# Kernel tuning notes

Hardware: AMD Instinct MI355X
Metric: run time of the kernel (lower is better)

## Reference

```python
import jax, jax.numpy as jnp
import numpy as np

B, T, D, H = 64, 256, 512, 512
COMB = D + H + D  # x, h, mask concatenated


def setup_inputs() -> dict:
    key = jax.random.key(0)
    ks = jax.random.split(key, 16)
    s = 1.0 / np.sqrt(COMB)
    sd = 1.0 / np.sqrt(D)
    inp = {
        "x": jax.random.normal(ks[0], (B, 4, T, D), dtype=jnp.float32),
        "X_mean": jax.random.normal(ks[1], (T, D), dtype=jnp.float32),
        # gate linears: stored as [in, out] so we do comb @ W + b
        "Wi": jax.random.uniform(ks[2], (COMB, H), minval=-s, maxval=s),
        "bi": jax.random.uniform(ks[3], (H,), minval=-s, maxval=s),
        "Wf": jax.random.uniform(ks[4], (COMB, H), minval=-s, maxval=s),
        "bf": jax.random.uniform(ks[5], (H,), minval=-s, maxval=s),
        "Wo": jax.random.uniform(ks[6], (COMB, H), minval=-s, maxval=s),
        "bo": jax.random.uniform(ks[7], (H,), minval=-s, maxval=s),
        "Wc": jax.random.uniform(ks[8], (COMB, H), minval=-s, maxval=s),
        "bc": jax.random.uniform(ks[9], (H,), minval=-s, maxval=s),
        # gamma_x_l: FilterLinear with identity filter -> diagonal weight + bias
        "gx_w": jax.random.uniform(ks[10], (D,), minval=-sd, maxval=sd),
        "gx_b": jax.random.uniform(ks[11], (D,), minval=-sd, maxval=sd),
        # gamma_h_l: full linear D -> D, stored [in, out]
        "gh_W": jax.random.uniform(ks[12], (D, D), minval=-sd, maxval=sd),
        "gh_b": jax.random.uniform(ks[13], (D,), minval=-sd, maxval=sd),
    }
    return inp


def _forward(x, X_mean, Wi, bi, Wf, bf, Wo, bo, Wc, bc, gx_w, gx_b, gh_W, gh_b):
    # split the packed input: each [T, B, D] for scan
    X = jnp.transpose(x[:, 0], (1, 0, 2))
    Xl = jnp.transpose(x[:, 1], (1, 0, 2))
    M = jnp.transpose(x[:, 2], (1, 0, 2))
    Dl = jnp.transpose(x[:, 3], (1, 0, 2))

    h0 = jnp.zeros((x.shape[0], H), dtype=x.dtype)
    c0 = jnp.zeros((x.shape[0], H), dtype=x.dtype)

    def step(carry, inp):
        h, c = carry
        xt, xl, m, dl, xm = inp  # xm: [D]
        delta_x = jnp.exp(-jnp.maximum(0.0, dl * gx_w + gx_b))
        delta_h = jnp.exp(-jnp.maximum(0.0, dl @ gh_W + gh_b))
        xt = m * xt + (1.0 - m) * (delta_x * xl + (1.0 - delta_x) * xm)
        h = delta_h * h
        comb = jnp.concatenate([xt, h, m], axis=-1)  # [B, COMB]
        i = jax.nn.sigmoid(comb @ Wi + bi)
        f = jax.nn.sigmoid(comb @ Wf + bf)
        o = jax.nn.sigmoid(comb @ Wo + bo)
        c_tilde = jnp.tanh(comb @ Wc + bc)
        c = f * c + i * c_tilde
        h = o * jnp.tanh(c)
        return (h, c), h

    _, outs = jax.lax.scan(step, (h0, c0), (X, Xl, M, Dl, X_mean))
    return jnp.transpose(outs, (1, 0, 2))  # [B, T, H]


def reference(x, X_mean, Wi, bi, Wf, bf, Wo, bo, Wc, bc, gx_w, gx_b, gh_W, gh_b):
    return _forward(x, X_mean, Wi, bi, Wf, bf, Wo, bo, Wc, bc, gx_w, gx_b, gh_W, gh_b)
```

## Files before the change

kernel.cpp:

```cpp
#include <hip/hip_runtime.h>
#include <hip/hip_fp16.h>
#include <math.h>

#define TT 256
#define BB 64
#define DD 512
#define HH 512
#define NC 2048

#define AH_OFF   0ull
#define DLH_OFF  8388608ull
#define DH_OFF   12582912ull
#define GP_OFF   20971520ull
#define WCT_OFF  37748736ull
#define GHT_OFF  38797312ull
#define WHT_OFF  38928384ull
#define BC_OFF   39452672ull
#define HS_OFF   39454720ull
#define FLG_OFF  39487488ull

typedef _Float16 h8_t __attribute__((ext_vector_type(8)));
typedef _Float16 h4_t __attribute__((ext_vector_type(4)));
typedef float f32x4 __attribute__((ext_vector_type(4)));
typedef unsigned long long ull2_t __attribute__((ext_vector_type(2)));

typedef const __attribute__((address_space(1))) void* gas_p;
typedef __attribute__((address_space(3))) void* las_p;

__device__ __forceinline__ float fast_exp2(float x) {
#if defined(__has_builtin)
#if __has_builtin(__builtin_amdgcn_exp2f)
  return __builtin_amdgcn_exp2f(x);
#else
  return exp2f(x);
#endif
#else
  return exp2f(x);
#endif
}
__device__ __forceinline__ float fast_rcp(float x) {
#if defined(__has_builtin)
#if __has_builtin(__builtin_amdgcn_rcpf)
  return __builtin_amdgcn_rcpf(x);
#else
  return 1.0f / x;
#endif
#else
  return 1.0f / x;
#endif
}
#define LOG2E 1.4426950408889634f
__device__ __forceinline__ float sigmoidf_(float v) {
  return fast_rcp(1.0f + fast_exp2(-LOG2E * v));
}
__device__ __forceinline__ float tanhf_(float v) {
  return 1.0f - 2.0f * fast_rcp(1.0f + fast_exp2(2.0f * LOG2E * v));
}

__global__ __launch_bounds__(256) void repack_kernel(
    const float* __restrict__ Wi, const float* __restrict__ bi,
    const float* __restrict__ Wf, const float* __restrict__ bff,
    const float* __restrict__ Wo, const float* __restrict__ bo,
    const float* __restrict__ Wc, const float* __restrict__ bc,
    const float* __restrict__ ghW,
    __half* __restrict__ WCT, __half* __restrict__ WHT,
    __half* __restrict__ GHT, float* __restrict__ BC) {
  int idx = blockIdx.x * 256 + threadIdx.x;
  int k = idx >> 9, j = idx & 511;
  const float* Ws[4] = {Wi, Wf, Wo, Wc};
  const float* bs[4] = {bi, bff, bo, bc};
#pragma unroll
  for (int g = 0; g < 4; ++g) {
    const float* W = Ws[g];
    int col = j * 4 + g;
    WCT[(size_t)col * 1024 + k] = __float2half(W[(size_t)k * 512 + j]);
    WCT[(size_t)col * 1024 + 512 + k] = __float2half(W[(size_t)(1024 + k) * 512 + j]);
    WHT[(size_t)col * 512 + k] = __float2half(W[(size_t)(512 + k) * 512 + j]);
    if (k == 0) BC[col] = bs[g][j];
  }
  GHT[(size_t)j * 512 + k] = __float2half(ghW[(size_t)k * 512 + j]);
}

__global__ __launch_bounds__(256) void xt_kernel(
    const float* __restrict__ x, const float* __restrict__ Xmean,
    const float* __restrict__ gxw, const float* __restrict__ gxb,
    __half* __restrict__ AH, __half* __restrict__ DLh) {
  int idx = blockIdx.x * 256 + threadIdx.x;
  int d = (idx & 127) * 4;
  int r = idx >> 7;
  int b = r & 63, t = r >> 6;
  size_t base = (((size_t)b * 4) * TT + t) * DD + d;
  const float4 X = *(const float4*)&x[base];
  const float4 Xl = *(const float4*)&x[base + (size_t)TT * DD];
  const float4 M = *(const float4*)&x[base + 2ull * TT * DD];
  const float4 Dl = *(const float4*)&x[base + 3ull * TT * DD];
  const float4 xm = *(const float4*)&Xmean[(size_t)t * DD + d];
  const float4 gw = *(const float4*)&gxw[d];
  const float4 gb = *(const float4*)&gxb[d];
  float o[4];
  {
    float dx = fast_exp2(-LOG2E * fmaxf(0.f, Dl.x * gw.x + gb.x));
    o[0] = M.x * X.x + (1.f - M.x) * (dx * Xl.x + (1.f - dx) * xm.x);
  }
  {
    float dx = fast_exp2(-LOG2E * fmaxf(0.f, Dl.y * gw.y + gb.y));
    o[1] = M.y * X.y + (1.f - M.y) * (dx * Xl.y + (1.f - dx) * xm.y);
  }
  {
    float dx = fast_exp2(-LOG2E * fmaxf(0.f, Dl.z * gw.z + gb.z));
    o[2] = M.z * X.z + (1.f - M.z) * (dx * Xl.z + (1.f - dx) * xm.z);
  }
  {
    float dx = fast_exp2(-LOG2E * fmaxf(0.f, Dl.w * gw.w + gb.w));
    o[3] = M.w * X.w + (1.f - M.w) * (dx * Xl.w + (1.f - dx) * xm.w);
  }
  h4_t xo = {(_Float16)o[0], (_Float16)o[1], (_Float16)o[2], (_Float16)o[3]};
  h4_t mo = {(_Float16)M.x, (_Float16)M.y, (_Float16)M.z, (_Float16)M.w};
  h4_t dlo = {(_Float16)Dl.x, (_Float16)Dl.y, (_Float16)Dl.z, (_Float16)Dl.w};
  *(h4_t*)&AH[(size_t)r * 1024 + d] = xo;
  *(h4_t*)&AH[(size_t)r * 1024 + 512 + d] = mo;
  *(h4_t*)&DLh[(size_t)r * 512 + d] = dlo;
}

__global__ __launch_bounds__(256, 2) void gemm16(
    const __half* __restrict__ A, const __half* __restrict__ BT,
    const float* __restrict__ bias, void* __restrict__ C,
    int K, int Ncols, int mode) {
  __shared__ _Float16 Ash[128 * 32];
  __shared__ _Float16 Bsh[128 * 32];
  const int tid = threadIdx.x;
  const int lane = tid & 63, w = tid >> 6;
  const int l15 = lane & 15, quad = lane >> 4;
  const int wr = w >> 1, wc = w & 1;
  const int row0 = blockIdx.y * 128, col0 = blockIdx.x * 128;

  f32x4 acc[4][4] = {};

  const int ci0 = tid, ci1 = 256 + tid;
  const int ar0 = ci0 >> 2, ac0 = (ci0 & 3) * 8;
  const int ar1 = ci1 >> 2, ac1 = (ci1 & 3) * 8;
  const __half* Abase = A + (size_t)row0 * K;
  const __half* Bbase = BT + (size_t)col0 * K;

  for (int k0 = 0; k0 < K; k0 += 32) {
    __syncthreads();
    __builtin_amdgcn_global_load_lds((gas_p)(Abase + (size_t)ar0 * K + k0 + ac0),
                                     (las_p)(Ash + ci0 * 8), 16, 0, 0);
    __builtin_amdgcn_global_load_lds((gas_p)(Abase + (size_t)ar1 * K + k0 + ac1),
                                     (las_p)(Ash + ci1 * 8), 16, 0, 0);
    __builtin_amdgcn_global_load_lds((gas_p)(Bbase + (size_t)ar0 * K + k0 + ac0),
                                     (las_p)(Bsh + ci0 * 8), 16, 0, 0);
    __builtin_amdgcn_global_load_lds((gas_p)(Bbase + (size_t)ar1 * K + k0 + ac1),
                                     (las_p)(Bsh + ci1 * 8), 16, 0, 0);
    __syncthreads();
    h8_t af[4], bf[4];
#pragma unroll
    for (int mt = 0; mt < 4; ++mt)
      af[mt] = *(const h8_t*)&Ash[(wr * 64 + mt * 16 + l15) * 32 + quad * 8];
#pragma unroll
    for (int ct = 0; ct < 4; ++ct)
      bf[ct] = *(const h8_t*)&Bsh[(wc * 64 + ct * 16 + l15) * 32 + quad * 8];
#pragma unroll
    for (int mt = 0; mt < 4; ++mt)
#pragma unroll
      for (int ct = 0; ct < 4; ++ct)
        acc[mt][ct] = __builtin_amdgcn_mfma_f32_16x16x32_f16(af[mt], bf[ct], acc[mt][ct], 0, 0, 0);
  }

#pragma unroll
  for (int ct = 0; ct < 4; ++ct) {
    const int col = col0 + wc * 64 + ct * 16 + l15;
    const float bv = bias[col];
#pragma unroll
    for (int mt = 0; mt < 4; ++mt) {
#pragma unroll
      for (int reg = 0; reg < 4; ++reg) {
        const int row = row0 + wr * 64 + mt * 16 + quad * 4 + reg;
        float v = acc[mt][ct][reg] + bv;
        if (mode == 0) {
          ((__half*)C)[(size_t)row * Ncols + col] = __float2half(v);
        } else {
          ((float*)C)[(size_t)row * Ncols + col] = fast_exp2(-LOG2E * fmaxf(0.f, v));
        }
      }
    }
  }
}

__global__ __launch_bounds__(512)
__attribute__((amdgpu_waves_per_eu(2, 2))) void persist_rnn(
    const __half* __restrict__ GPh, const float* __restrict__ DH,
    const __half* __restrict__ WHT, unsigned* __restrict__ hs,
    int* __restrict__ flg, float* __restrict__ out) {
  __shared__ __align__(16) float gbuf[16 * 260];
  __shared__ __align__(16) unsigned long long stag[2048];
  const int g = blockIdx.x & 3;
  const int m = blockIdx.x >> 2;
  const int tid = threadIdx.x;
  const int lane = tid & 63;
  const int w = tid >> 6;
  const int l15 = lane & 15;
  const int quad = lane >> 4;
  const int rowg0 = g << 4;

  h8_t bfrag[2][16];
  const int colbase = (m << 8) + (w << 5);
#pragma unroll
  for (int nt = 0; nt < 2; ++nt) {
#pragma unroll
    for (int kt = 0; kt < 16; ++kt) {
      int col = colbase + nt * 16 + l15;
      int k = kt * 32 + quad * 8;
      bfrag[nt][kt] = *(const h8_t*)&WHT[(size_t)col * 512 + k];
    }
  }

  const int r_ep = w;
  const int ug = (m << 6) + lane;
  const int ktu = ug >> 5, q3 = (ug >> 3) & 3, qi = (ug & 7) >> 1;
  const int d0 = ktu * 256 + (q3 * 16 + r_ep) * 4 + qi;
  const int d1 = ktu * 256 + (q3 * 16 + r_ep + 8) * 4 + qi;

  float c0 = 0.f, c1 = 0.f;

  for (int t = 0; t < TT; ++t) {
    const h4_t gha = *(const h4_t*)&GPh[((size_t)t * 64 + rowg0 + r_ep) * NC + (ug << 2)];
    const h4_t ghb = *(const h4_t*)&GPh[((size_t)t * 64 + rowg0 + r_ep + 8) * NC + (ug << 2)];
    const int tn = (t + 1 < TT) ? t + 1 : t;
    const float dha = DH[((size_t)tn * 64 + rowg0 + r_ep) * HH + ug];
    const float dhb = DH[((size_t)tn * 64 + rowg0 + r_ep + 8) * HH + ug];

    if (t > 0) {
      if (w == 0) {
        const int* fb = flg + (g << 3);
        for (;;) {
          int v = __hip_atomic_load(&fb[lane & 7], __ATOMIC_RELAXED,
                                    __HIP_MEMORY_SCOPE_AGENT);
          if (__all(v >= t)) break;
          __builtin_amdgcn_s_sleep(1);
        }
      }
      __syncthreads();
    }

    const unsigned long long* hsp =
        (const unsigned long long*)hs + ((size_t)(t & 1) * 4 + g) * 2048;
    unsigned long long sv0 = __hip_atomic_load(&hsp[tid], __ATOMIC_RELAXED,
                                               __HIP_MEMORY_SCOPE_AGENT);
    unsigned long long sv1 = __hip_atomic_load(&hsp[tid + 512], __ATOMIC_RELAXED,
                                               __HIP_MEMORY_SCOPE_AGENT);
    unsigned long long sv2 = __hip_atomic_load(&hsp[tid + 1024], __ATOMIC_RELAXED,
                                               __HIP_MEMORY_SCOPE_AGENT);
    unsigned long long sv3 = __hip_atomic_load(&hsp[tid + 1536], __ATOMIC_RELAXED,
                                               __HIP_MEMORY_SCOPE_AGENT);
    stag[tid] = sv0;
    stag[tid + 512] = sv1;
    stag[tid + 1024] = sv2;
    stag[tid + 1536] = sv3;
    __syncthreads();

    h8_t af[16];
#pragma unroll
    for (int kt = 0; kt < 16; ++kt) {
      ull2_t u2 = *(const ull2_t*)&stag[kt * 128 + lane * 2];
      af[kt] = __builtin_bit_cast(h8_t, u2);
    }

    f32x4 acc0 = {0.f, 0.f, 0.f, 0.f};
    f32x4 acc1 = {0.f, 0.f, 0.f, 0.f};
#pragma unroll
    for (int kt = 0; kt < 16; ++kt) {
      acc0 = __builtin_amdgcn_mfma_f32_16x16x32_f16(af[kt], bfrag[0][kt], acc0, 0, 0, 0);
      acc1 = __builtin_amdgcn_mfma_f32_16x16x32_f16(af[kt], bfrag[1][kt], acc1, 0, 0, 0);
    }
#pragma unroll
    for (int reg = 0; reg < 4; ++reg) {
      int row = quad * 4 + reg;
      gbuf[row * 260 + (w << 5) + l15] = acc0[reg];
      gbuf[row * 260 + (w << 5) + 16 + l15] = acc1[reg];
    }
    __syncthreads();

    float h0v, h1v;
    {
      const float4 gv = *(const float4*)&gbuf[r_ep * 260 + (lane << 2)];
      float ig = sigmoidf_(gv.x + (float)gha[0]);
      float fg = sigmoidf_(gv.y + (float)gha[1]);
      float og = sigmoidf_(gv.z + (float)gha[2]);
      float ct = tanhf_(gv.w + (float)gha[3]);
      c0 = fg * c0 + ig * ct;
      h0v = og * tanhf_(c0);
    }
    {
      const float4 gv = *(const float4*)&gbuf[(r_ep + 8) * 260 + (lane << 2)];
      float ig = sigmoidf_(gv.x + (float)ghb[0]);
      float fg = sigmoidf_(gv.y + (float)ghb[1]);
      float og = sigmoidf_(gv.z + (float)ghb[2]);
      float ct = tanhf_(gv.w + (float)ghb[3]);
      c1 = fg * c1 + ig * ct;
      h1v = og * tanhf_(c1);
    }

    if (t + 1 < TT) {
      unsigned* hsn = hs + ((size_t)((t + 1) & 1) * 4 + g) * 4096;
      unsigned short hb0 = __half_as_ushort(__float2half(dha * h0v));
      unsigned o0 = (unsigned)__shfl_xor((int)(unsigned)hb0, 1) & 0xffffu;
      unsigned short hb1 = __half_as_ushort(__float2half(dhb * h1v));
      unsigned o1 = (unsigned)__shfl_xor((int)(unsigned)hb1, 1) & 0xffffu;
      if (!(lane & 1)) {
        __hip_atomic_store(&hsn[d0], (unsigned)hb0 | (o0 << 16), __ATOMIC_RELAXED,
                           __HIP_MEMORY_SCOPE_AGENT);
        __hip_atomic_store(&hsn[d1], (unsigned)hb1 | (o1 << 16), __ATOMIC_RELAXED,
                           __HIP_MEMORY_SCOPE_AGENT);
      }
    }
    out[((size_t)(rowg0 + r_ep) * TT + t) * HH + ug] = h0v;
    out[((size_t)(rowg0 + r_ep + 8) * TT + t) * HH + ug] = h1v;

    __syncthreads();
    if (t + 1 < TT && tid == 0)
      __hip_atomic_store(&flg[(g << 3) + m], t + 1, __ATOMIC_RELAXED,
                         __HIP_MEMORY_SCOPE_AGENT);
  }
}

extern "C" void kernel_launch(void* const* d_in, const int* in_sizes, int n_in,
                              void* d_out, int out_size, void* d_ws,
                              size_t ws_size, hipStream_t stream) {
  const float* x = (const float*)d_in[0];
  const float* Xmean = (const float*)d_in[1];
  const float* Wi = (const float*)d_in[2];
  const float* bi = (const float*)d_in[3];
  const float* Wf = (const float*)d_in[4];
  const float* bf = (const float*)d_in[5];
  const float* Wo = (const float*)d_in[6];
  const float* bo = (const float*)d_in[7];
  const float* Wc = (const float*)d_in[8];
  const float* bc = (const float*)d_in[9];
  const float* gxw = (const float*)d_in[10];
  const float* gxb = (const float*)d_in[11];
  const float* ghW = (const float*)d_in[12];
  const float* ghb = (const float*)d_in[13];
  float* out = (float*)d_out;
  float* ws = (float*)d_ws;

  __half* AH = (__half*)(ws + AH_OFF);
  __half* DLh = (__half*)(ws + DLH_OFF);
  float* DH = ws + DH_OFF;
  __half* GPh = (__half*)(ws + GP_OFF);
  __half* WCT = (__half*)(ws + WCT_OFF);
  __half* GHT = (__half*)(ws + GHT_OFF);
  __half* WHT = (__half*)(ws + WHT_OFF);
  float* BC = ws + BC_OFF;
  unsigned* HS = (unsigned*)(ws + HS_OFF);
  int* FLG = (int*)(ws + FLG_OFF);

  hipMemsetAsync(HS, 0, (2ull * 4 * 4096 + 64) * sizeof(unsigned), stream);

  repack_kernel<<<1024, 256, 0, stream>>>(Wi, bi, Wf, bf, Wo, bo, Wc, bc, ghW,
                                          WCT, WHT, GHT, BC);
  xt_kernel<<<8192, 256, 0, stream>>>(x, Xmean, gxw, gxb, AH, DLh);
  gemm16<<<dim3(4, 128), 256, 0, stream>>>(DLh, GHT, ghb, (void*)DH, 512, 512, 1);
  gemm16<<<dim3(16, 128), 256, 0, stream>>>(AH, WCT, BC, (void*)GPh, 1024, NC, 0);

  void* args[] = {(void*)&GPh, (void*)&DH, (void*)&WHT,
                  (void*)&HS, (void*)&FLG, (void*)&out};
  hipLaunchCooperativeKernel((const void*)persist_rnn, dim3(32), dim3(512),
                             args, 0, stream);
}
```

Baseline: 1.046 ms.

## Use 16 blocks of 1024 threads for persistent RNN to cut cross-block syncs

Changes the persistent recurrent kernel from 32 blocks of 512 threads to 16 blocks of 1024 threads. Each block now owns twice as many gate columns, so every step waits on 4 peer flags instead of 8 and each block stages h with two loads per thread instead of four. The column mapping, LDS gate buffer stride and flag indexing are changed to match. In exchange there are fewer CUs doing the per-step work, and the larger block has less register headroom per thread, with the risk of spills.

```diff
diff --git a/kernel.cpp b/kernel.cpp
--- a/kernel.cpp
+++ b/kernel.cpp
@@ -187,12 +187,11 @@
   }
 }
 
-__global__ __launch_bounds__(512)
-__attribute__((amdgpu_waves_per_eu(2, 2))) void persist_rnn(
+__global__ __launch_bounds__(1024, 4) void persist_rnn(
     const __half* __restrict__ GPh, const float* __restrict__ DH,
     const __half* __restrict__ WHT, unsigned* __restrict__ hs,
     int* __restrict__ flg, float* __restrict__ out) {
-  __shared__ __align__(16) float gbuf[16 * 260];
+  __shared__ __align__(16) float gbuf[16 * 516];
   __shared__ __align__(16) unsigned long long stag[2048];
   const int g = blockIdx.x & 3;
   const int m = blockIdx.x >> 2;
@@ -204,7 +203,7 @@
   const int rowg0 = g << 4;
 
   h8_t bfrag[2][16];
-  const int colbase = (m << 8) + (w << 5);
+  const int colbase = (m << 9) + (w << 5);
 #pragma unroll
   for (int nt = 0; nt < 2; ++nt) {
 #pragma unroll
@@ -215,26 +214,27 @@
     }
   }
 
-  const int r_ep = w;
-  const int ug = (m << 6) + lane;
-  const int ktu = ug >> 5, q3 = (ug >> 3) & 3, qi = (ug & 7) >> 1;
-  const int d0 = ktu * 256 + (q3 * 16 + r_ep) * 4 + qi;
-  const int d1 = ktu * 256 + (q3 * 16 + r_ep + 8) * 4 + qi;
+  const int r0 = w & 7;
+  const int hsub = ((w >> 3) << 6) + lane;
+  const int ugh = (m << 7) + hsub;
+  const int ktu = ugh >> 5, q3 = (ugh >> 3) & 3, qi = (ugh & 7) >> 1;
+  const int d0 = ktu * 256 + (q3 * 16 + r0) * 4 + qi;
+  const int d1 = ktu * 256 + (q3 * 16 + r0 + 8) * 4 + qi;
 
   float c0 = 0.f, c1 = 0.f;
 
   for (int t = 0; t < TT; ++t) {
-    const h4_t gha = *(const h4_t*)&GPh[((size_t)t * 64 + rowg0 + r_ep) * NC + (ug << 2)];
-    const h4_t ghb = *(const h4_t*)&GPh[((size_t)t * 64 + rowg0 + r_ep + 8) * NC + (ug << 2)];
+    const h4_t gha = *(const h4_t*)&GPh[((size_t)t * 64 + rowg0 + r0) * NC + (ugh << 2)];
+    const h4_t ghb = *(const h4_t*)&GPh[((size_t)t * 64 + rowg0 + r0 + 8) * NC + (ugh << 2)];
     const int tn = (t + 1 < TT) ? t + 1 : t;
-    const float dha = DH[((size_t)tn * 64 + rowg0 + r_ep) * HH + ug];
-    const float dhb = DH[((size_t)tn * 64 + rowg0 + r_ep + 8) * HH + ug];
+    const float dha = DH[((size_t)tn * 64 + rowg0 + r0) * HH + ugh];
+    const float dhb = DH[((size_t)tn * 64 + rowg0 + r0 + 8) * HH + ugh];
 
     if (t > 0) {
       if (w == 0) {
-        const int* fb = flg + (g << 3);
+        const int* fb = flg + (g << 4);
         for (;;) {
-          int v = __hip_atomic_load(&fb[lane & 7], __ATOMIC_RELAXED,
+          int v = __hip_atomic_load(&fb[lane & 3], __ATOMIC_RELAXED,
                                     __HIP_MEMORY_SCOPE_AGENT);
           if (__all(v >= t)) break;
           __builtin_amdgcn_s_sleep(1);
@@ -247,16 +247,10 @@
         (const unsigned long long*)hs + ((size_t)(t & 1) * 4 + g) * 2048;
     unsigned long long sv0 = __hip_atomic_load(&hsp[tid], __ATOMIC_RELAXED,
                                                __HIP_MEMORY_SCOPE_AGENT);
-    unsigned long long sv1 = __hip_atomic_load(&hsp[tid + 512], __ATOMIC_RELAXED,
-                                               __HIP_MEMORY_SCOPE_AGENT);
-    unsigned long long sv2 = __hip_atomic_load(&hsp[tid + 1024], __ATOMIC_RELAXED,
-                                               __HIP_MEMORY_SCOPE_AGENT);
-    unsigned long long sv3 = __hip_atomic_load(&hsp[tid + 1536], __ATOMIC_RELAXED,
+    unsigned long long sv1 = __hip_atomic_load(&hsp[tid + 1024], __ATOMIC_RELAXED,
                                                __HIP_MEMORY_SCOPE_AGENT);
     stag[tid] = sv0;
-    stag[tid + 512] = sv1;
-    stag[tid + 1024] = sv2;
-    stag[tid + 1536] = sv3;
+    stag[tid + 1024] = sv1;
     __syncthreads();
 
     h8_t af[16];
@@ -276,14 +270,14 @@
 #pragma unroll
     for (int reg = 0; reg < 4; ++reg) {
       int row = quad * 4 + reg;
-      gbuf[row * 260 + (w << 5) + l15] = acc0[reg];
-      gbuf[row * 260 + (w << 5) + 16 + l15] = acc1[reg];
+      gbuf[row * 516 + (w << 5) + l15] = acc0[reg];
+      gbuf[row * 516 + (w << 5) + 16 + l15] = acc1[reg];
     }
     __syncthreads();
 
     float h0v, h1v;
     {
-      const float4 gv = *(const float4*)&gbuf[r_ep * 260 + (lane << 2)];
+      const float4 gv = *(const float4*)&gbuf[r0 * 516 + (hsub << 2)];
       float ig = sigmoidf_(gv.x + (float)gha[0]);
       float fg = sigmoidf_(gv.y + (float)gha[1]);
       float og = sigmoidf_(gv.z + (float)gha[2]);
@@ -292,7 +286,7 @@
       h0v = og * tanhf_(c0);
     }
     {
-      const float4 gv = *(const float4*)&gbuf[(r_ep + 8) * 260 + (lane << 2)];
+      const float4 gv = *(const float4*)&gbuf[(r0 + 8) * 516 + (hsub << 2)];
       float ig = sigmoidf_(gv.x + (float)ghb[0]);
       float fg = sigmoidf_(gv.y + (float)ghb[1]);
       float og = sigmoidf_(gv.z + (float)ghb[2]);
@@ -314,12 +308,12 @@
                            __HIP_MEMORY_SCOPE_AGENT);
       }
     }
-    out[((size_t)(rowg0 + r_ep) * TT + t) * HH + ug] = h0v;
-    out[((size_t)(rowg0 + r_ep + 8) * TT + t) * HH + ug] = h1v;
+    out[((size_t)(rowg0 + r0) * TT + t) * HH + ugh] = h0v;
+    out[((size_t)(rowg0 + r0 + 8) * TT + t) * HH + ugh] = h1v;
 
     __syncthreads();
     if (t + 1 < TT && tid == 0)
-      __hip_atomic_store(&flg[(g << 3) + m], t + 1, __ATOMIC_RELAXED,
+      __hip_atomic_store(&flg[(g << 4) + m], t + 1, __ATOMIC_RELAXED,
                          __HIP_MEMORY_SCOPE_AGENT);
   }
 }
@@ -365,6 +359,6 @@
 
   void* args[] = {(void*)&GPh, (void*)&DH, (void*)&WHT,
                   (void*)&HS, (void*)&FLG, (void*)&out};
-  hipLaunchCooperativeKernel((const void*)persist_rnn, dim3(32), dim3(512),
+  hipLaunchCooperativeKernel((const void*)persist_rnn, dim3(16), dim3(1024),
                              args, 0, stream);
 }
```

Measured after the change: 2.284 ms. 118% more time.
